# Kernel optimization log

Hardware: AMD Instinct MI355X
Metric: run time of the kernel (lower is better)

The kernel has to match this reference:

```python
import jax, jax.numpy as jnp
import numpy as np

N = 100000      # nodes
E = 1600000     # edges
F_IN, H1, H2, H3, F_OUT = 64, 128, 128, 64, 8


def _lin(key, fan_in, fan_out):
    return jax.random.normal(key, (fan_in, fan_out), jnp.float32) / np.sqrt(fan_in).astype(np.float32)


def setup_inputs() -> dict:
    key = jax.random.key(0)
    ks = jax.random.split(key, 16)
    x = jax.random.normal(ks[0], (N, F_IN), jnp.float32)
    edge_index = jax.random.randint(ks[1], (2, E), 0, N, dtype=jnp.int64)
    return {
        "x": x,
        "edge_index": edge_index,
        "eps1": jnp.zeros((), jnp.float32),
        "eps2": jnp.zeros((), jnp.float32),
        "eps3": jnp.zeros((), jnp.float32),
        "W1a": _lin(ks[2], F_IN, H1), "b1a": jnp.zeros((H1,), jnp.float32),
        "W1b": _lin(ks[3], H1, H1),   "b1b": jnp.zeros((H1,), jnp.float32),
        "W2a": _lin(ks[4], H1, H2),   "b2a": jnp.zeros((H2,), jnp.float32),
        "W2b": _lin(ks[5], H2, H2),   "b2b": jnp.zeros((H2,), jnp.float32),
        "W3a": _lin(ks[6], H2, H3),   "b3a": jnp.zeros((H3,), jnp.float32),
        "W3b": _lin(ks[7], H3, H3),   "b3b": jnp.zeros((H3,), jnp.float32),
        "Wfc": _lin(ks[8], H3, F_OUT), "bfc": jnp.zeros((F_OUT,), jnp.float32),
    }


def _gin_conv(x, src, dst, eps, Wa, ba, Wb, bb):
    # out_i = MLP((1+eps) * x_i + sum_{j in N(i)} x_j)
    agg = jax.ops.segment_sum(x[src], dst, num_segments=N)  # scatter-add over edges
    h = (1.0 + eps) * x + agg
    return jax.nn.relu(h @ Wa + ba) @ Wb + bb


def reference(x, edge_index, eps1, eps2, eps3,
              W1a, b1a, W1b, b1b,
              W2a, b2a, W2b, b2b,
              W3a, b3a, W3b, b3b,
              Wfc, bfc):
    src, dst = edge_index[0], edge_index[1]
    x = jax.nn.relu(_gin_conv(x, src, dst, eps1, W1a, b1a, W1b, b1b))
    x = jax.nn.relu(_gin_conv(x, src, dst, eps2, W2a, b2a, W2b, b2b))
    x = jax.nn.relu(_gin_conv(x, src, dst, eps3, W3a, b3a, W3b, b3b))
    emb = jax.lax.stop_gradient(x)  # x.clone().detach()
    out = x @ Wfc + bfc
    return out, emb
```

## Files before the change

kernel.cpp:

```cpp
#include <hip/hip_runtime.h>
#include <hip/hip_bf16.h>
#include <stdint.h>

typedef unsigned short ushort_t;
typedef __attribute__((ext_vector_type(8))) short short8;
typedef __attribute__((ext_vector_type(4))) float floatx4;
typedef __attribute__((ext_vector_type(2))) float floatx2;

__device__ __forceinline__ unsigned short f2bf(float f){
  union { float f; unsigned int i; } v; v.f = f;
  unsigned int r = v.i + 0x7FFFu + ((v.i >> 16) & 1u);
  return (unsigned short)(r >> 16);
}
__device__ __forceinline__ unsigned int pack2(unsigned short lo, unsigned short hi){
  return ((unsigned int)hi << 16) | (unsigned int)lo;
}
__device__ __forceinline__ floatx2 bfpair(unsigned int v){
  union { unsigned int u; float f; } lo, hi;
  lo.u = v << 16; hi.u = v & 0xffff0000u;
  floatx2 r; r.x = lo.f; r.y = hi.f; return r;
}


__global__ __launch_bounds__(256)
void k_prep(const unsigned int* __restrict__ w, int* __restrict__ ghist, int E, int N, int nbB,
            const float2* __restrict__ xin, unsigned int* __restrict__ xb, int total2, int tobfB,
            const float* __restrict__ W1a, const float* __restrict__ W1b, const float* __restrict__ W2a,
            const float* __restrict__ W2b, const float* __restrict__ W3a, const float* __restrict__ W3b,
            const float* __restrict__ Wfc, ushort_t* __restrict__ wout,
            ushort_t* __restrict__ xbz, ushort_t* __restrict__ x1z, ushort_t* __restrict__ ybz)
{
  int b = blockIdx.x, t = threadIdx.x;
  if (b < nbB){
    __shared__ int h[256];
    __shared__ unsigned int dred[4];
    h[t] = 0;
    int base = b*4096 + t;
    unsigned int acc = 0;
    #pragma unroll
    for (int i=0;i<16;++i){
      int e = base + i*256;
      if (e < E) acc |= w[2*e+1];
    }
    #pragma unroll
    for (int o=32;o>=1;o>>=1) acc |= __shfl_xor(acc, o);
    if ((t&63)==0) dred[t>>6] = acc;
    __syncthreads();
    int m = (dred[0]|dred[1]|dred[2]|dred[3]) != 0;
    #pragma unroll
    for (int i=0;i<16;++i){
      int e = base + i*256;
      if (e < E){
        int d = m ? (int)w[(size_t)E + e] : (int)w[2*((size_t)E + e)];
        if ((unsigned)d < (unsigned)N) atomicAdd(&h[d>>9], 1);
      }
    }
    __syncthreads();
    if (h[t]) atomicAdd(&ghist[t], h[t]);
  } else if (b < nbB + tobfB){
    int i = (b - nbB)*256 + t;
    if (i < total2){
      float2 v = xin[i];
      xb[i] = pack2(f2bf(v.x), f2bf(v.y));
    }
  } else {
    int id = (b - nbB - tobfB)*256 + t;
    if (id >= 74752){
      int id2 = id - 74752;
      if      (id2 <  64) xbz[id2]      = 0;
      else if (id2 < 192) x1z[id2-64]   = 0;
      else if (id2 < 256) ybz[id2-192]  = 0;
      return;
    }
    const float* src; int K, M, base2, local;
    if      (id <  8192){ src=W1a; K=64;  M=128; base2=0;     local=id; }
    else if (id < 24576){ src=W1b; K=128; M=128; base2=8192;  local=id-8192; }
    else if (id < 40960){ src=W2a; K=128; M=128; base2=24576; local=id-24576; }
    else if (id < 57344){ src=W2b; K=128; M=128; base2=40960; local=id-40960; }
    else if (id < 65536){ src=W3a; K=128; M=64;  base2=57344; local=id-57344; }
    else if (id < 69632){ src=W3b; K=64;  M=64;  base2=65536; local=id-65536; }
    else if (id < 70656){ src=Wfc; K=64;  M=16;  base2=69632; local=id-69632; }
    else                { src=nullptr; K=64; M=64; base2=70656; local=id-70656; }
    int k = local / M, nn = local - k*M;
    float val;
    if (src == nullptr) val = (k == nn) ? 1.0f : 0.0f;
    else if (src == Wfc) val = (nn<8) ? Wfc[k*8+nn] : 0.0f;
    else                 val = src[k*M+nn];
    int idx = (((nn>>4)*(K/32) + (k>>5))*4 + ((k>>3)&3))*128 + (nn&15)*8 + (k&7);
    wout[base2+idx] = f2bf(val);
  }
}


__global__ __launch_bounds__(256) void k_bin(const unsigned int* __restrict__ w,
                                             const int* __restrict__ ghist, int* __restrict__ gcur,
                                             int2* __restrict__ pairs,
                                             int E, int N, int NB){
  __shared__ int sv[256];
  __shared__ int h[256];
  __shared__ int cur[256];
  __shared__ unsigned int dred[4];
  int t = threadIdx.x;
  int gv = ghist[t];
  sv[t] = gv; __syncthreads();
  for (int o=1;o<256;o<<=1){
    int xv = (t>=o)? sv[t-o] : 0;
    __syncthreads();
    sv[t] += xv;
    __syncthreads();
  }
  int excl = sv[t] - gv;

  h[t] = 0;
  int base = blockIdx.x*4096 + t;
  unsigned int acc = 0;
  #pragma unroll
  for (int i=0;i<16;++i){
    int e = base + i*256;
    if (e < E) acc |= w[2*e+1];
  }
  #pragma unroll
  for (int o=32;o>=1;o>>=1) acc |= __shfl_xor(acc, o);
  if ((t&63)==0) dred[t>>6] = acc;
  __syncthreads();
  int m = (dred[0]|dred[1]|dred[2]|dred[3]) != 0;
  int d[16], s[16];
  #pragma unroll
  for (int i=0;i<16;++i){
    int e = base + i*256;
    d[i] = -1; s[i] = 0;
    if (e < E){
      if (m){ s[i] = (int)w[e];           d[i] = (int)w[(size_t)E + e]; }
      else  { s[i] = (int)w[2*(size_t)e]; d[i] = (int)w[2*((size_t)E + e)]; }
      if ((unsigned)d[i] >= (unsigned)N || (unsigned)s[i] >= (unsigned)N) d[i] = -1;
    }
  }
  #pragma unroll
  for (int i=0;i<16;++i)
    if (d[i] >= 0) atomicAdd(&h[d[i]>>9], 1);
  __syncthreads();
  if (t < NB && h[t]) cur[t] = excl + atomicAdd(&gcur[t], h[t]);
  __syncthreads();
  #pragma unroll
  for (int i=0;i<16;++i){
    if (d[i] >= 0){
      int p = atomicAdd(&cur[d[i]>>9], 1);
      pairs[p] = make_int2(d[i], s[i]);
    }
  }
}

__global__ __launch_bounds__(256) void k_bcsr(const int2* __restrict__ pairs, const int* __restrict__ ghist,
                                              int* __restrict__ offs, int* __restrict__ csr, int N, int NB){
  __shared__ int sv[256];
  __shared__ int cnt[512];
  __shared__ int wsum[4];
  int b = blockIdx.x, t = threadIdx.x, lane = t&63, wv = t>>6;
  int gv = ghist[t];
  sv[t] = gv; __syncthreads();
  for (int o=1;o<256;o<<=1){
    int xv = (t>=o)? sv[t-o] : 0;
    __syncthreads();
    sv[t] += xv;
    __syncthreads();
  }
  int lo = (b==0) ? 0 : sv[b-1];
  int hi = sv[b];
  int node0 = b << 9;
  cnt[t] = 0; cnt[t+256] = 0;
  __syncthreads();
  for (int i = lo+t; i < hi; i += 256){
    int2 p = pairs[i];
    atomicAdd(&cnt[p.x - node0], 1);
  }
  __syncthreads();
  int v0 = cnt[2*t], v1 = cnt[2*t+1], tot = v0+v1;
  int s = tot;
  #pragma unroll
  for (int o=1;o<64;o<<=1){ int xv = __shfl_up(s,o); if (lane>=o) s += xv; }
  if (lane==63) wsum[wv] = s;
  __syncthreads();
  int basev = 0;
  for (int j=0;j<wv;++j) basev += wsum[j];
  int excl = basev + s - tot;
  int e0 = lo + excl, e1 = lo + excl + v0;
  cnt[2*t] = e0; cnt[2*t+1] = e1;
  int n0 = node0 + 2*t, n1 = node0 + 2*t + 1;
  if (n0 < N) offs[n0] = e0;
  if (n1 < N) offs[n1] = e1;
  if (b == NB-1 && t == 255) offs[N] = hi;
  __syncthreads();
  for (int i = lo+t; i < hi; i += 256){
    int2 p = pairs[i];
    int pos = atomicAdd(&cnt[p.x - node0], 1);
    csr[pos] = p.y;
  }
}


template<int F>
__global__ __launch_bounds__(256) void k_gatherx(const uint4* __restrict__ xr, const int* __restrict__ offs,
                                                 const int* __restrict__ csr, const float* __restrict__ epsp,
                                                 uint4* __restrict__ hr, int n, int nzrow){
  constexpr int RS  = F/8;
  constexpr int LPN = 4*RS;
  constexpr int NPW = 64/LPN;
  constexpr int CH  = LPN;
  constexpr int MAXG = CH/16;
  int gt = blockIdx.x*256 + threadIdx.x;
  int wv = gt >> 6, lane = gt & 63;
  int grp = lane / LPN;
  int lin = lane % LPN;
  int q   = lin / RS;
  int f   = lin % RS;
  int node = wv*NPW + grp;
  if (node >= n) return;
  const size_t row = (size_t)node*RS;
  float e1s = 1.0f + epsp[0];
  floatx2 a0,a1,a2,a3;
  if (q == 0){
    uint4 sv = xr[row + f];
    floatx2 es; es.x = e1s; es.y = e1s;
    a0 = es*bfpair(sv.x); a1 = es*bfpair(sv.y);
    a2 = es*bfpair(sv.z); a3 = es*bfpair(sv.w);
  } else {
    floatx2 z; z.x = 0.f; z.y = 0.f;
    a0 = z; a1 = z; a2 = z; a3 = z;
  }
  int u0 = offs[node], u1 = offs[node+1];
  int deg = u1 - u0;

#define ISSUE(g, V0,V1,V2,V3) { int bb = grp*LPN + (g)*16 + q; \
    int s0=__shfl(cv,bb), s1=__shfl(cv,bb+4), s2=__shfl(cv,bb+8), s3=__shfl(cv,bb+12); \
    V0 = xr[(size_t)s0*RS + f]; V1 = xr[(size_t)s1*RS + f]; \
    V2 = xr[(size_t)s2*RS + f]; V3 = xr[(size_t)s3*RS + f]; }
#define ACCV(V)  { a0 += bfpair((V).x); a1 += bfpair((V).y); a2 += bfpair((V).z); a3 += bfpair((V).w); }
#define ACC4(V0,V1,V2,V3) { ACCV(V0) ACCV(V1) ACCV(V2) ACCV(V3) }

  for (int c0 = 0; c0 < deg; c0 += CH){
    int rem = deg - c0;
    int cv = nzrow;
    if (lin < rem) cv = csr[u0 + c0 + lin];
    int nk = rem < CH ? rem : CH;
    int ng = (nk + 15) >> 4;
    uint4 A0,A1,A2,A3, B0,B1,B2,B3;
    ISSUE(0, A0,A1,A2,A3)
    if (ng > 1) { ISSUE(1, B0,B1,B2,B3) }
    ACC4(A0,A1,A2,A3)
    if (ng > 1){
      if constexpr (MAXG >= 3) { if (ng > 2) ISSUE(2, A0,A1,A2,A3) }
      ACC4(B0,B1,B2,B3)
      if constexpr (MAXG >= 3){
        if (ng > 2){
          if (ng > 3) { ISSUE(3, B0,B1,B2,B3) }
          ACC4(A0,A1,A2,A3)
          if (ng > 3) { ACC4(B0,B1,B2,B3) }
        }
      }
    }
  }
#undef ISSUE
#undef ACCV
#undef ACC4
#define RED(av) { av.x += __shfl_xor(av.x, RS);   av.y += __shfl_xor(av.y, RS); \
                  av.x += __shfl_xor(av.x, 2*RS); av.y += __shfl_xor(av.y, 2*RS); }
  RED(a0) RED(a1) RED(a2) RED(a3)
#undef RED
  if (q == 0){
    uint4 o;
    o.x = pack2(f2bf(a0.x), f2bf(a0.y));
    o.y = pack2(f2bf(a1.x), f2bf(a1.y));
    o.z = pack2(f2bf(a2.x), f2bf(a2.y));
    o.w = pack2(f2bf(a3.x), f2bf(a3.y));
    hr[row + f] = o;
  }
}


template<int F, int M1, int M2, bool LAST, bool Y3>
__global__ __launch_bounds__(256)
void k_gmlp(const uint4* __restrict__ xr, const int* __restrict__ offs,
            const int* __restrict__ csr, const float* __restrict__ epsp,
            const ushort_t* __restrict__ wp1, const float* __restrict__ b1,
            const ushort_t* __restrict__ wp2, const float* __restrict__ b2,
            ushort_t* __restrict__ xout,
            float* __restrict__ embp,
            const ushort_t* __restrict__ wpfc, const float* __restrict__ bfc,
            float* __restrict__ outp, int n)
{
  constexpr int RS  = F/8;
  constexpr int LPN = 4*RS;
  constexpr int NPW = 64/LPN;
  constexpr int CH  = LPN;
  constexpr int MAXG = CH/16;
  constexpr int NPR = 4*NPW;
  constexpr int PADC = F + 8;
  constexpr int NT1 = M1/16, NT2 = M2/16, KC1 = F/32, KC2 = M1/32;

  __shared__ short sH[64*PADC] __attribute__((aligned(16)));
  __shared__ short sC1[4*(M1/8)*136];
  __shared__ short sX3[LAST ? (4*8*136) : 1];

  int tid = threadIdx.x, lane = tid&63, w = tid>>6;
  int node0 = blockIdx.x*64;

  {
    int grp = lane / LPN;
    int lin = lane % LPN;
    int q   = lin / RS;
    int f   = lin % RS;
    float e1s = 1.0f + epsp[0];
    #pragma unroll
    for (int rd = 0; rd < 64/NPR; ++rd){
      int lrow = rd*NPR + w*NPW + grp;
      int node = node0 + lrow;
      int nd = node < n ? node : n;
      floatx2 a0,a1,a2,a3;
      if (q == 0){
        uint4 sv = xr[(size_t)nd*RS + f];
        floatx2 es; es.x = e1s; es.y = e1s;
        a0 = es*bfpair(sv.x); a1 = es*bfpair(sv.y);
        a2 = es*bfpair(sv.z); a3 = es*bfpair(sv.w);
      } else {
        floatx2 z; z.x = 0.f; z.y = 0.f;
        a0 = z; a1 = z; a2 = z; a3 = z;
      }
      int u0 = 0, deg = 0;
      if (node < n){ u0 = offs[node]; deg = offs[node+1] - u0; }

#define ISSUE(g, V0,V1,V2,V3) { int bb = grp*LPN + (g)*16 + q; \
    int s0=__shfl(cv,bb), s1=__shfl(cv,bb+4), s2=__shfl(cv,bb+8), s3=__shfl(cv,bb+12); \
    V0 = xr[(size_t)s0*RS + f]; V1 = xr[(size_t)s1*RS + f]; \
    V2 = xr[(size_t)s2*RS + f]; V3 = xr[(size_t)s3*RS + f]; }
#define ACCV(V)  { a0 += bfpair((V).x); a1 += bfpair((V).y); a2 += bfpair((V).z); a3 += bfpair((V).w); }
#define ACC4(V0,V1,V2,V3) { ACCV(V0) ACCV(V1) ACCV(V2) ACCV(V3) }
      for (int c0 = 0; c0 < deg; c0 += CH){
        int rem = deg - c0;
        int cv = n;
        if (lin < rem) cv = csr[u0 + c0 + lin];
        int nk = rem < CH ? rem : CH;
        int ng = (nk + 15) >> 4;
        uint4 A0,A1,A2,A3, B0,B1,B2,B3;
        ISSUE(0, A0,A1,A2,A3)
        if (ng > 1) { ISSUE(1, B0,B1,B2,B3) }
        ACC4(A0,A1,A2,A3)
        if (ng > 1){
          if constexpr (MAXG >= 3) { if (ng > 2) ISSUE(2, A0,A1,A2,A3) }
          ACC4(B0,B1,B2,B3)
          if constexpr (MAXG >= 3){
            if (ng > 2){
              if (ng > 3) { ISSUE(3, B0,B1,B2,B3) }
              ACC4(A0,A1,A2,A3)
              if (ng > 3) { ACC4(B0,B1,B2,B3) }
            }
          }
        }
      }
#undef ISSUE
#undef ACCV
#undef ACC4
#define RED(av) { av.x += __shfl_xor(av.x, RS);   av.y += __shfl_xor(av.y, RS); \
                  av.x += __shfl_xor(av.x, 2*RS); av.y += __shfl_xor(av.y, 2*RS); }
      RED(a0) RED(a1) RED(a2) RED(a3)
#undef RED
      if (q == 0){
        uint4 o;
        o.x = pack2(f2bf(a0.x), f2bf(a0.y));
        o.y = pack2(f2bf(a1.x), f2bf(a1.y));
        o.z = pack2(f2bf(a2.x), f2bf(a2.y));
        o.w = pack2(f2bf(a3.x), f2bf(a3.y));
        *(uint4*)&sH[lrow*PADC + f*8] = o;
      }
    }
  }
  __syncthreads();

  int m16 = lane&15, quad = lane>>4;
  int row0 = node0 + w*16;

  floatx4 acc[NT1];
  #pragma unroll
  for (int i=0;i<NT1;++i) acc[i] = (floatx4){0.f,0.f,0.f,0.f};
  #pragma unroll
  for (int kc=0; kc<KC1; ++kc){
    short8 a = *(const short8*)&sH[(w*16 + m16)*PADC + kc*32 + quad*8];
    #pragma unroll
    for (int nt=0; nt<NT1; ++nt){
      short8 b = *(const short8*)(wp1 + (size_t)((nt*KC1+kc)*64 + lane)*8);
      acc[nt] = __builtin_amdgcn_mfma_f32_16x16x32_bf16(a, b, acc[nt], 0, 0, 0);
    }
  }
  #pragma unroll
  for (int nt=0; nt<NT1; ++nt){
    int c = nt*16 + m16;
    float bias = b1[c];
    #pragma unroll
    for (int r=0;r<4;++r){
      float v = fmaxf(acc[nt][r] + bias, 0.f);
      int mm = quad*4 + r;
      sC1[(w*(M1/8) + (c>>3))*136 + mm*8 + (c&7)] = (short)f2bf(v);
    }
  }
  __syncthreads();

  floatx4 acc2[NT2];
  #pragma unroll
  for (int i=0;i<NT2;++i) acc2[i] = (floatx4){0.f,0.f,0.f,0.f};
  #pragma unroll
  for (int kc=0; kc<KC2; ++kc){
    short8 a = *(const short8*)&sC1[(w*(M1/8) + kc*4 + quad)*136 + m16*8];
    #pragma unroll
    for (int nt=0; nt<NT2; ++nt){
      short8 b = *(const short8*)(wp2 + (size_t)((nt*KC2+kc)*64 + lane)*8);
      acc2[nt] = __builtin_amdgcn_mfma_f32_16x16x32_bf16(a, b, acc2[nt], 0, 0, 0);
    }
  }
  #pragma unroll
  for (int nt=0; nt<NT2; ++nt){
    int c = nt*16 + m16;
    float bias = b2[c];
    #pragma unroll
    for (int r=0;r<4;++r){
      float v = fmaxf(acc2[nt][r] + bias, 0.f);
      int mm = quad*4 + r;
      int row = row0 + mm;
      if constexpr (Y3){
        sC1[(w*(M2/8) + (c>>3))*136 + mm*8 + (c&7)] = (short)f2bf(v);
      } else if constexpr (!LAST){
        if (row < n) xout[(size_t)row*M2 + c] = f2bf(v);
      } else {
        if (row < n) embp[(size_t)row*64 + c] = v;
        sX3[(w*8 + (c>>3))*136 + mm*8 + (c&7)] = (short)f2bf(v);
      }
    }
  }

  if constexpr (Y3){
    constexpr int KC3 = M2/32;
    floatx4 acc3[4];
    #pragma unroll
    for (int i=0;i<4;++i) acc3[i] = (floatx4){0.f,0.f,0.f,0.f};
    #pragma unroll
    for (int kc=0; kc<KC3; ++kc){
      short8 a = *(const short8*)&sC1[(w*(M2/8) + kc*4 + quad)*136 + m16*8];
      #pragma unroll
      for (int nt=0; nt<4; ++nt){
        short8 b = *(const short8*)(wpfc + (size_t)((nt*KC3+kc)*64 + lane)*8);
        acc3[nt] = __builtin_amdgcn_mfma_f32_16x16x32_bf16(a, b, acc3[nt], 0, 0, 0);
      }
    }
    #pragma unroll
    for (int nt=0; nt<4; ++nt){
      int c = nt*16 + m16;
      #pragma unroll
      for (int r=0;r<4;++r){
        int row = row0 + quad*4 + r;
        if (row < n) xout[(size_t)row*64 + c] = f2bf(acc3[nt][r]);
      }
    }
  }

  if constexpr (LAST){
    __syncthreads();
    floatx4 accf = (floatx4){0.f,0.f,0.f,0.f};
    #pragma unroll
    for (int kc=0; kc<2; ++kc){
      short8 a = *(const short8*)&sX3[(w*8 + kc*4 + quad)*136 + m16*8];
      short8 b = *(const short8*)(wpfc + (size_t)(kc*64 + lane)*8);
      accf = __builtin_amdgcn_mfma_f32_16x16x32_bf16(a, b, accf, 0, 0, 0);
    }
    if (m16 < 8){
      float bias = bfc[m16];
      #pragma unroll
      for (int r=0;r<4;++r){
        int row = row0 + quad*4 + r;
        if (row < n) outp[(size_t)row*8 + m16] = accf[r] + bias;
      }
    }
  }
}


template<int F, int M1, int M2, bool LAST, bool Y3>
__global__ __launch_bounds__(256)
void k_mlp(const ushort_t* __restrict__ h,
           const ushort_t* __restrict__ wp1, const float* __restrict__ b1,
           const ushort_t* __restrict__ wp2, const float* __restrict__ b2,
           ushort_t* __restrict__ xout,
           float* __restrict__ embp,
           const ushort_t* __restrict__ wpfc, const float* __restrict__ bfc,
           float* __restrict__ outp, int n)
{
  constexpr int NT1 = M1/16, NT2 = M2/16, KC1 = F/32, KC2 = M1/32;
  __shared__ short sC1[4*(M1/8)*136];
  __shared__ short sX3[LAST ? (4*8*136) : 1];
  int tid = threadIdx.x, lane = tid&63, w = tid>>6;
  int m16 = lane&15, quad = lane>>4;
  int row0 = blockIdx.x*64 + w*16;
  size_t arow = (size_t)(row0 + m16);

  floatx4 acc[NT1];
  #pragma unroll
  for (int i=0;i<NT1;++i) acc[i] = (floatx4){0.f,0.f,0.f,0.f};
  #pragma unroll
  for (int kc=0; kc<KC1; ++kc){
    short8 a = *(const short8*)(h + arow*F + kc*32 + quad*8);
    #pragma unroll
    for (int nt=0; nt<NT1; ++nt){
      short8 b = *(const short8*)(wp1 + (size_t)((nt*KC1+kc)*64 + lane)*8);
      acc[nt] = __builtin_amdgcn_mfma_f32_16x16x32_bf16(a, b, acc[nt], 0, 0, 0);
    }
  }
  #pragma unroll
  for (int nt=0; nt<NT1; ++nt){
    int c = nt*16 + m16;
    float bias = b1[c];
    #pragma unroll
    for (int r=0;r<4;++r){
      float v = fmaxf(acc[nt][r] + bias, 0.f);
      int mm = quad*4 + r;
      sC1[(w*(M1/8) + (c>>3))*136 + mm*8 + (c&7)] = (short)f2bf(v);
    }
  }
  __syncthreads();

  floatx4 acc2[NT2];
  #pragma unroll
  for (int i=0;i<NT2;++i) acc2[i] = (floatx4){0.f,0.f,0.f,0.f};
  #pragma unroll
  for (int kc=0; kc<KC2; ++kc){
    short8 a = *(const short8*)&sC1[(w*(M1/8) + kc*4 + quad)*136 + m16*8];
    #pragma unroll
    for (int nt=0; nt<NT2; ++nt){
      short8 b = *(const short8*)(wp2 + (size_t)((nt*KC2+kc)*64 + lane)*8);
      acc2[nt] = __builtin_amdgcn_mfma_f32_16x16x32_bf16(a, b, acc2[nt], 0, 0, 0);
    }
  }
  #pragma unroll
  for (int nt=0; nt<NT2; ++nt){
    int c = nt*16 + m16;
    float bias = b2[c];
    #pragma unroll
    for (int r=0;r<4;++r){
      float v = fmaxf(acc2[nt][r] + bias, 0.f);
      int mm = quad*4 + r;
      int row = row0 + mm;
      if constexpr (Y3){
        sC1[(w*(M2/8) + (c>>3))*136 + mm*8 + (c&7)] = (short)f2bf(v);
      } else if constexpr (!LAST){
        if (row < n) xout[(size_t)row*M2 + c] = f2bf(v);
      } else {
        if (row < n) embp[(size_t)row*64 + c] = v;
        sX3[(w*8 + (c>>3))*136 + mm*8 + (c&7)] = (short)f2bf(v);
      }
    }
  }

  if constexpr (Y3){
    constexpr int KC3 = M2/32;
    floatx4 acc3[4];
    #pragma unroll
    for (int i=0;i<4;++i) acc3[i] = (floatx4){0.f,0.f,0.f,0.f};
    #pragma unroll
    for (int kc=0; kc<KC3; ++kc){
      short8 a = *(const short8*)&sC1[(w*(M2/8) + kc*4 + quad)*136 + m16*8];
      #pragma unroll
      for (int nt=0; nt<4; ++nt){
        short8 b = *(const short8*)(wpfc + (size_t)((nt*KC3+kc)*64 + lane)*8);
        acc3[nt] = __builtin_amdgcn_mfma_f32_16x16x32_bf16(a, b, acc3[nt], 0, 0, 0);
      }
    }
    #pragma unroll
    for (int nt=0; nt<4; ++nt){
      int c = nt*16 + m16;
      #pragma unroll
      for (int r=0;r<4;++r){
        int row = row0 + quad*4 + r;
        if (row < n) xout[(size_t)row*64 + c] = f2bf(acc3[nt][r]);
      }
    }
  }

  if constexpr (LAST){
    __syncthreads();
    floatx4 accf = (floatx4){0.f,0.f,0.f,0.f};
    #pragma unroll
    for (int kc=0; kc<2; ++kc){
      short8 a = *(const short8*)&sX3[(w*8 + kc*4 + quad)*136 + m16*8];
      short8 b = *(const short8*)(wpfc + (size_t)(kc*64 + lane)*8);
      accf = __builtin_amdgcn_mfma_f32_16x16x32_bf16(a, b, accf, 0, 0, 0);
    }
    if (m16 < 8){
      float bias = bfc[m16];
      #pragma unroll
      for (int r=0;r<4;++r){
        int row = row0 + quad*4 + r;
        if (row < n) outp[(size_t)row*8 + m16] = accf[r] + bias;
      }
    }
  }
}


extern "C" void kernel_launch(void* const* d_in, const int* in_sizes, int n_in,
                              void* d_out, int out_size, void* d_ws, size_t ws_size,
                              hipStream_t stream)
{
  const int N = in_sizes[0] / 64;
  const int E = in_sizes[1] / 2;
  const int NB = (N + 511) / 512;
  const float*        x    = (const float*)d_in[0];
  const unsigned int* ew   = (const unsigned int*)d_in[1];
  const float* eps1 = (const float*)d_in[2];
  const float* eps2 = (const float*)d_in[3];
  const float* eps3 = (const float*)d_in[4];
  const float* W1a  = (const float*)d_in[5];
  const float* b1a  = (const float*)d_in[6];
  const float* W1b  = (const float*)d_in[7];
  const float* b1b  = (const float*)d_in[8];
  const float* W2a  = (const float*)d_in[9];
  const float* b2a  = (const float*)d_in[10];
  const float* W2b  = (const float*)d_in[11];
  const float* b2b  = (const float*)d_in[12];
  const float* W3a  = (const float*)d_in[13];
  const float* b3a  = (const float*)d_in[14];
  const float* W3b  = (const float*)d_in[15];
  const float* b3b  = (const float*)d_in[16];
  const float* Wfc  = (const float*)d_in[17];
  const float* bfc  = (const float*)d_in[18];

  float* outp = (float*)d_out;
  float* emb  = outp + (size_t)N*8;

  const int Npad = ((N + 63)/64)*64;

  char* ws = (char*)d_ws;
  size_t o = 0;
  auto alloc = [&](size_t bytes)->char* {
    char* p = ws + o;
    o = (o + bytes + 255) & ~(size_t)255;
    return p;
  };
  int*      ghist = (int*)alloc(512*4);
  int*      gcur  = ghist + 256;
  int*      offs  = (int*)alloc((size_t)(N+1)*4);
  int2*     pairs = (int2*)alloc((size_t)E*8);
  int*      csr   = (int*)alloc((size_t)E*4);
  ushort_t* wperm = (ushort_t*)alloc(74752ull*2);
  ushort_t* xb    = (ushort_t*)alloc(((size_t)Npad + 64)*64*2);
  ushort_t* hbuf  = (ushort_t*)alloc((size_t)Npad*128*2);
  ushort_t* x1    = (ushort_t*)alloc(((size_t)Npad + 64)*128*2);
  ushort_t* ybuf  = (ushort_t*)alloc(((size_t)Npad + 64)*64*2);

  hipMemsetAsync(ghist, 0, 512*4, stream);
  const int nbB   = (E + 4095)/4096;
  const int tobfB = (N*32 + 255)/256;
  const int permB = (74752 + 256 + 255)/256;
  k_prep<<<nbB + tobfB + permB, 256, 0, stream>>>(ew, ghist, E, N, nbB,
                                                  (const float2*)x, (unsigned int*)xb, N*32, tobfB,
                                                  W1a, W1b, W2a, W2b, W3a, W3b, Wfc, wperm,
                                                  xb + (size_t)N*64, x1 + (size_t)N*128, ybuf + (size_t)N*64);
  k_bin<<<nbB, 256, 0, stream>>>(ew, ghist, gcur, pairs, E, N, NB);
  k_bcsr<<<NB, 256, 0, stream>>>(pairs, ghist, offs, csr, N, NB);

  k_gmlp<64,128,128,false,false><<<Npad/64, 256, 0, stream>>>((const uint4*)xb, offs, csr, eps1,
                                                              wperm+0, b1a, wperm+8192, b1b,
                                                              x1, nullptr, nullptr, nullptr, nullptr, N);
  k_gatherx<128><<<(N+3)/4, 256, 0, stream>>>((const uint4*)x1, offs, csr, eps2,
                                              (uint4*)hbuf, N, N);
  k_mlp<128,128,128,false,true><<<Npad/64, 256, 0, stream>>>(hbuf, wperm+24576, b2a, wperm+40960, b2b,
                                                             ybuf, nullptr, wperm+57344, nullptr, nullptr, N);
  k_gmlp<64,64,64,true,false><<<Npad/64, 256, 0, stream>>>((const uint4*)ybuf, offs, csr, eps3,
                                                           wperm+70656, b3a, wperm+65536, b3b,
                                                           nullptr, emb, wperm+69632, bfc, outp, N);
}
```

Baseline: 360.5 us.

## Pack CSR build pairs into 32-bit words and widen preprocessing blocks to 1024

Each edge is now packed as the node's local offset within its bin plus the source index in one 32-bit word, replacing an int2 and halving pairs traffic. The prep, bin and CSR kernels move to 1024-thread blocks. The prep kernel records the index-layout flag per block so the bin kernel does not recompute it. The gather+MLP kernel now shares one shared-memory buffer across its stages, loads A fragments into registers before a barrier, and drops the unused Y3 path. The packing assumes node indices fit in 17 bits, and the larger blocks change occupancy and the number of scan barriers.

Result: faster. 345.2 us (-4.2%).

```diff
diff --git a/kernel.cpp b/kernel.cpp
--- a/kernel.cpp
+++ b/kernel.cpp
@@ -22,8 +22,9 @@
 }
 
 
-__global__ __launch_bounds__(256)
-void k_prep(const unsigned int* __restrict__ w, int* __restrict__ ghist, int E, int N, int nbB,
+__global__ __launch_bounds__(1024)
+void k_prep(const unsigned int* __restrict__ w, int* __restrict__ ghist, int* __restrict__ dflag,
+            int E, int N, int nbB,
             const float2* __restrict__ xin, unsigned int* __restrict__ xb, int total2, int tobfB,
             const float* __restrict__ W1a, const float* __restrict__ W1b, const float* __restrict__ W2a,
             const float* __restrict__ W2b, const float* __restrict__ W3a, const float* __restrict__ W3b,
@@ -33,38 +34,42 @@
   int b = blockIdx.x, t = threadIdx.x;
   if (b < nbB){
     __shared__ int h[256];
-    __shared__ unsigned int dred[4];
-    h[t] = 0;
+    __shared__ unsigned int dred[16];
+    if (t < 256) h[t] = 0;
     int base = b*4096 + t;
     unsigned int acc = 0;
     #pragma unroll
-    for (int i=0;i<16;++i){
-      int e = base + i*256;
+    for (int i=0;i<4;++i){
+      int e = base + i*1024;
       if (e < E) acc |= w[2*e+1];
     }
     #pragma unroll
     for (int o=32;o>=1;o>>=1) acc |= __shfl_xor(acc, o);
     if ((t&63)==0) dred[t>>6] = acc;
     __syncthreads();
-    int m = (dred[0]|dred[1]|dred[2]|dred[3]) != 0;
-    #pragma unroll
-    for (int i=0;i<16;++i){
-      int e = base + i*256;
+    unsigned int mm = 0;
+    #pragma unroll
+    for (int i=0;i<16;++i) mm |= dred[i];
+    int m = mm != 0;
+    if (t == 0) dflag[b] = m;
+    #pragma unroll
+    for (int i=0;i<4;++i){
+      int e = base + i*1024;
       if (e < E){
         int d = m ? (int)w[(size_t)E + e] : (int)w[2*((size_t)E + e)];
         if ((unsigned)d < (unsigned)N) atomicAdd(&h[d>>9], 1);
       }
     }
     __syncthreads();
-    if (h[t]) atomicAdd(&ghist[t], h[t]);
+    if (t < 256 && h[t]) atomicAdd(&ghist[t], h[t]);
   } else if (b < nbB + tobfB){
-    int i = (b - nbB)*256 + t;
+    int i = (b - nbB)*1024 + t;
     if (i < total2){
       float2 v = xin[i];
       xb[i] = pack2(f2bf(v.x), f2bf(v.y));
     }
   } else {
-    int id = (b - nbB - tobfB)*256 + t;
+    int id = (b - nbB - tobfB)*1024 + t;
     if (id >= 74752){
       int id2 = id - 74752;
       if      (id2 <  64) xbz[id2]      = 0;
@@ -92,42 +97,33 @@
 }
 
 
-__global__ __launch_bounds__(256) void k_bin(const unsigned int* __restrict__ w,
-                                             const int* __restrict__ ghist, int* __restrict__ gcur,
-                                             int2* __restrict__ pairs,
-                                             int E, int N, int NB){
+__global__ __launch_bounds__(1024) void k_bin(const unsigned int* __restrict__ w,
+                                              const int* __restrict__ ghist, const int* __restrict__ dflag,
+                                              int* __restrict__ gcur,
+                                              unsigned int* __restrict__ pairs,
+                                              int E, int N, int NB){
   __shared__ int sv[256];
   __shared__ int h[256];
   __shared__ int cur[256];
-  __shared__ unsigned int dred[4];
   int t = threadIdx.x;
-  int gv = ghist[t];
-  sv[t] = gv; __syncthreads();
+  int gv = 0;
+  if (t < 256){ gv = ghist[t]; sv[t] = gv; }
+  __syncthreads();
   for (int o=1;o<256;o<<=1){
-    int xv = (t>=o)? sv[t-o] : 0;
-    __syncthreads();
-    sv[t] += xv;
-    __syncthreads();
-  }
-  int excl = sv[t] - gv;
-
-  h[t] = 0;
+    int xv = (t>=o && t<256)? sv[t-o] : 0;
+    __syncthreads();
+    if (t < 256) sv[t] += xv;
+    __syncthreads();
+  }
+  int excl = (t < 256) ? sv[t] - gv : 0;
+  if (t < 256) h[t] = 0;
+  int m = dflag[blockIdx.x];
   int base = blockIdx.x*4096 + t;
-  unsigned int acc = 0;
-  #pragma unroll
-  for (int i=0;i<16;++i){
-    int e = base + i*256;
-    if (e < E) acc |= w[2*e+1];
-  }
-  #pragma unroll
-  for (int o=32;o>=1;o>>=1) acc |= __shfl_xor(acc, o);
-  if ((t&63)==0) dred[t>>6] = acc;
-  __syncthreads();
-  int m = (dred[0]|dred[1]|dred[2]|dred[3]) != 0;
-  int d[16], s[16];
-  #pragma unroll
-  for (int i=0;i<16;++i){
-    int e = base + i*256;
+  __syncthreads();
+  int d[4], s[4];
+  #pragma unroll
+  for (int i=0;i<4;++i){
+    int e = base + i*1024;
     d[i] = -1; s[i] = 0;
     if (e < E){
       if (m){ s[i] = (int)w[e];           d[i] = (int)w[(size_t)E + e]; }
@@ -136,64 +132,69 @@
     }
   }
   #pragma unroll
-  for (int i=0;i<16;++i)
+  for (int i=0;i<4;++i)
     if (d[i] >= 0) atomicAdd(&h[d[i]>>9], 1);
   __syncthreads();
   if (t < NB && h[t]) cur[t] = excl + atomicAdd(&gcur[t], h[t]);
   __syncthreads();
   #pragma unroll
-  for (int i=0;i<16;++i){
+  for (int i=0;i<4;++i){
     if (d[i] >= 0){
       int p = atomicAdd(&cur[d[i]>>9], 1);
-      pairs[p] = make_int2(d[i], s[i]);
-    }
-  }
-}
-
-__global__ __launch_bounds__(256) void k_bcsr(const int2* __restrict__ pairs, const int* __restrict__ ghist,
-                                              int* __restrict__ offs, int* __restrict__ csr, int N, int NB){
+      pairs[p] = ((unsigned int)(d[i] & 511) << 17) | (unsigned int)s[i];
+    }
+  }
+}
+
+__global__ __launch_bounds__(1024) void k_bcsr(const unsigned int* __restrict__ pairs, const int* __restrict__ ghist,
+                                               int* __restrict__ offs, int* __restrict__ csr, int N, int NB){
   __shared__ int sv[256];
   __shared__ int cnt[512];
   __shared__ int wsum[4];
   int b = blockIdx.x, t = threadIdx.x, lane = t&63, wv = t>>6;
-  int gv = ghist[t];
-  sv[t] = gv; __syncthreads();
+  if (t < 256) sv[t] = ghist[t];
+  __syncthreads();
   for (int o=1;o<256;o<<=1){
-    int xv = (t>=o)? sv[t-o] : 0;
-    __syncthreads();
-    sv[t] += xv;
+    int xv = (t>=o && t<256)? sv[t-o] : 0;
+    __syncthreads();
+    if (t < 256) sv[t] += xv;
     __syncthreads();
   }
   int lo = (b==0) ? 0 : sv[b-1];
   int hi = sv[b];
   int node0 = b << 9;
-  cnt[t] = 0; cnt[t+256] = 0;
-  __syncthreads();
-  for (int i = lo+t; i < hi; i += 256){
-    int2 p = pairs[i];
-    atomicAdd(&cnt[p.x - node0], 1);
-  }
-  __syncthreads();
-  int v0 = cnt[2*t], v1 = cnt[2*t+1], tot = v0+v1;
-  int s = tot;
-  #pragma unroll
-  for (int o=1;o<64;o<<=1){ int xv = __shfl_up(s,o); if (lane>=o) s += xv; }
-  if (lane==63) wsum[wv] = s;
-  __syncthreads();
-  int basev = 0;
-  for (int j=0;j<wv;++j) basev += wsum[j];
-  int excl = basev + s - tot;
-  int e0 = lo + excl, e1 = lo + excl + v0;
-  cnt[2*t] = e0; cnt[2*t+1] = e1;
-  int n0 = node0 + 2*t, n1 = node0 + 2*t + 1;
-  if (n0 < N) offs[n0] = e0;
-  if (n1 < N) offs[n1] = e1;
+  if (t < 512) cnt[t] = 0;
+  __syncthreads();
+  for (int i = lo+t; i < hi; i += 1024){
+    unsigned int p = pairs[i];
+    atomicAdd(&cnt[p >> 17], 1);
+  }
+  __syncthreads();
+  int v0 = 0, v1 = 0, tot = 0, s = 0;
+  if (t < 256){
+    v0 = cnt[2*t]; v1 = cnt[2*t+1]; tot = v0+v1;
+    s = tot;
+    #pragma unroll
+    for (int o=1;o<64;o<<=1){ int xv = __shfl_up(s,o); if (lane>=o) s += xv; }
+    if (lane==63) wsum[wv] = s;
+  }
+  __syncthreads();
+  if (t < 256){
+    int basev = 0;
+    for (int j=0;j<wv;++j) basev += wsum[j];
+    int excl = basev + s - tot;
+    int e0 = lo + excl, e1 = lo + excl + v0;
+    cnt[2*t] = e0; cnt[2*t+1] = e1;
+    int n0 = node0 + 2*t, n1 = node0 + 2*t + 1;
+    if (n0 < N) offs[n0] = e0;
+    if (n1 < N) offs[n1] = e1;
+  }
   if (b == NB-1 && t == 255) offs[N] = hi;
   __syncthreads();
-  for (int i = lo+t; i < hi; i += 256){
-    int2 p = pairs[i];
-    int pos = atomicAdd(&cnt[p.x - node0], 1);
-    csr[pos] = p.y;
+  for (int i = lo+t; i < hi; i += 1024){
+    unsigned int p = pairs[i];
+    int pos = atomicAdd(&cnt[p >> 17], 1);
+    csr[pos] = (int)(p & 0x1FFFFu);
   }
 }
 
@@ -277,7 +278,7 @@
 }
 
 
-template<int F, int M1, int M2, bool LAST, bool Y3>
+template<int F, int M1, int M2, bool LAST>
 __global__ __launch_bounds__(256)
 void k_gmlp(const uint4* __restrict__ xr, const int* __restrict__ offs,
             const int* __restrict__ csr, const float* __restrict__ epsp,
@@ -296,10 +297,15 @@
   constexpr int NPR = 4*NPW;
   constexpr int PADC = F + 8;
   constexpr int NT1 = M1/16, NT2 = M2/16, KC1 = F/32, KC2 = M1/32;
-
-  __shared__ short sH[64*PADC] __attribute__((aligned(16)));
-  __shared__ short sC1[4*(M1/8)*136];
-  __shared__ short sX3[LAST ? (4*8*136) : 1];
+  static_assert(KC1 == 2, "a-frag preload written for KC1==2");
+  constexpr int SC1_SZ = 4*(M1/8)*136;
+  constexpr int SX3_SZ = LAST ? (4*8*136) : 0;
+  constexpr int UNION_SZ = (64*PADC > SC1_SZ + SX3_SZ) ? 64*PADC : (SC1_SZ + SX3_SZ);
+
+  __shared__ short sU[UNION_SZ] __attribute__((aligned(16)));
+  short* sH  = sU;
+  short* sC1 = sU;
+  short* sX3 = sU + SC1_SZ;
 
   int tid = threadIdx.x, lane = tid&63, w = tid>>6;
   int node0 = blockIdx.x*64;
@@ -377,18 +383,19 @@
 
   int m16 = lane&15, quad = lane>>4;
   int row0 = node0 + w*16;
+  short8 aR0 = *(const short8*)&sH[(w*16 + m16)*PADC + 0*32 + quad*8];
+  short8 aR1 = *(const short8*)&sH[(w*16 + m16)*PADC + 1*32 + quad*8];
+  __syncthreads();
 
   floatx4 acc[NT1];
   #pragma unroll
   for (int i=0;i<NT1;++i) acc[i] = (floatx4){0.f,0.f,0.f,0.f};
   #pragma unroll
-  for (int kc=0; kc<KC1; ++kc){
-    short8 a = *(const short8*)&sH[(w*16 + m16)*PADC + kc*32 + quad*8];
-    #pragma unroll
-    for (int nt=0; nt<NT1; ++nt){
-      short8 b = *(const short8*)(wp1 + (size_t)((nt*KC1+kc)*64 + lane)*8);
-      acc[nt] = __builtin_amdgcn_mfma_f32_16x16x32_bf16(a, b, acc[nt], 0, 0, 0);
-    }
+  for (int nt=0; nt<NT1; ++nt){
+    short8 b0 = *(const short8*)(wp1 + (size_t)((nt*KC1+0)*64 + lane)*8);
+    acc[nt] = __builtin_amdgcn_mfma_f32_16x16x32_bf16(aR0, b0, acc[nt], 0, 0, 0);
+    short8 b1v = *(const short8*)(wp1 + (size_t)((nt*KC1+1)*64 + lane)*8);
+    acc[nt] = __builtin_amdgcn_mfma_f32_16x16x32_bf16(aR1, b1v, acc[nt], 0, 0, 0);
   }
   #pragma unroll
   for (int nt=0; nt<NT1; ++nt){
@@ -424,38 +431,11 @@
       float v = fmaxf(acc2[nt][r] + bias, 0.f);
       int mm = quad*4 + r;
       int row = row0 + mm;
-      if constexpr (Y3){
-        sC1[(w*(M2/8) + (c>>3))*136 + mm*8 + (c&7)] = (short)f2bf(v);
-      } else if constexpr (!LAST){
+      if constexpr (!LAST){
         if (row < n) xout[(size_t)row*M2 + c] = f2bf(v);
       } else {
         if (row < n) embp[(size_t)row*64 + c] = v;
         sX3[(w*8 + (c>>3))*136 + mm*8 + (c&7)] = (short)f2bf(v);
-      }
-    }
-  }
-
-  if constexpr (Y3){
-    constexpr int KC3 = M2/32;
-    floatx4 acc3[4];
-    #pragma unroll
-    for (int i=0;i<4;++i) acc3[i] = (floatx4){0.f,0.f,0.f,0.f};
-    #pragma unroll
-    for (int kc=0; kc<KC3; ++kc){
-      short8 a = *(const short8*)&sC1[(w*(M2/8) + kc*4 + quad)*136 + m16*8];
-      #pragma unroll
-      for (int nt=0; nt<4; ++nt){
-        short8 b = *(const short8*)(wpfc + (size_t)((nt*KC3+kc)*64 + lane)*8);
-        acc3[nt] = __builtin_amdgcn_mfma_f32_16x16x32_bf16(a, b, acc3[nt], 0, 0, 0);
-      }
-    }
-    #pragma unroll
-    for (int nt=0; nt<4; ++nt){
-      int c = nt*16 + m16;
-      #pragma unroll
-      for (int r=0;r<4;++r){
-        int row = row0 + quad*4 + r;
-        if (row < n) xout[(size_t)row*64 + c] = f2bf(acc3[nt][r]);
       }
     }
   }
@@ -633,6 +613,7 @@
   float* emb  = outp + (size_t)N*8;
 
   const int Npad = ((N + 63)/64)*64;
+  const int nbB  = (E + 4095)/4096;
 
   char* ws = (char*)d_ws;
   size_t o = 0;
@@ -643,8 +624,9 @@
   };
   int*      ghist = (int*)alloc(512*4);
   int*      gcur  = ghist + 256;
+  int*      dflag = (int*)alloc((size_t)nbB*4);
   int*      offs  = (int*)alloc((size_t)(N+1)*4);
-  int2*     pairs = (int2*)alloc((size_t)E*8);
+  unsigned int* pairs = (unsigned int*)alloc((size_t)E*4);
   int*      csr   = (int*)alloc((size_t)E*4);
   ushort_t* wperm = (ushort_t*)alloc(74752ull*2);
   ushort_t* xb    = (ushort_t*)alloc(((size_t)Npad + 64)*64*2);
@@ -653,24 +635,23 @@
   ushort_t* ybuf  = (ushort_t*)alloc(((size_t)Npad + 64)*64*2);
 
   hipMemsetAsync(ghist, 0, 512*4, stream);
-  const int nbB   = (E + 4095)/4096;
-  const int tobfB = (N*32 + 255)/256;
-  const int permB = (74752 + 256 + 255)/256;
-  k_prep<<<nbB + tobfB + permB, 256, 0, stream>>>(ew, ghist, E, N, nbB,
-                                                  (const float2*)x, (unsigned int*)xb, N*32, tobfB,
-                                                  W1a, W1b, W2a, W2b, W3a, W3b, Wfc, wperm,
-                                                  xb + (size_t)N*64, x1 + (size_t)N*128, ybuf + (size_t)N*64);
-  k_bin<<<nbB, 256, 0, stream>>>(ew, ghist, gcur, pairs, E, N, NB);
-  k_bcsr<<<NB, 256, 0, stream>>>(pairs, ghist, offs, csr, N, NB);
-
-  k_gmlp<64,128,128,false,false><<<Npad/64, 256, 0, stream>>>((const uint4*)xb, offs, csr, eps1,
-                                                              wperm+0, b1a, wperm+8192, b1b,
-                                                              x1, nullptr, nullptr, nullptr, nullptr, N);
+  const int tobfB = (N*32 + 1023)/1024;
+  const int permB = (74752 + 256 + 1023)/1024;
+  k_prep<<<nbB + tobfB + permB, 1024, 0, stream>>>(ew, ghist, dflag, E, N, nbB,
+                                                   (const float2*)x, (unsigned int*)xb, N*32, tobfB,
+                                                   W1a, W1b, W2a, W2b, W3a, W3b, Wfc, wperm,
+                                                   xb + (size_t)N*64, x1 + (size_t)N*128, ybuf + (size_t)N*64);
+  k_bin<<<nbB, 1024, 0, stream>>>(ew, ghist, dflag, gcur, pairs, E, N, NB);
+  k_bcsr<<<NB, 1024, 0, stream>>>(pairs, ghist, offs, csr, N, NB);
+
+  k_gmlp<64,128,128,false><<<Npad/64, 256, 0, stream>>>((const uint4*)xb, offs, csr, eps1,
+                                                        wperm+0, b1a, wperm+8192, b1b,
+                                                        x1, nullptr, nullptr, nullptr, nullptr, N);
   k_gatherx<128><<<(N+3)/4, 256, 0, stream>>>((const uint4*)x1, offs, csr, eps2,
                                               (uint4*)hbuf, N, N);
   k_mlp<128,128,128,false,true><<<Npad/64, 256, 0, stream>>>(hbuf, wperm+24576, b2a, wperm+40960, b2b,
                                                              ybuf, nullptr, wperm+57344, nullptr, nullptr, N);
-  k_gmlp<64,64,64,true,false><<<Npad/64, 256, 0, stream>>>((const uint4*)ybuf, offs, csr, eps3,
-                                                           wperm+70656, b3a, wperm+65536, b3b,
-                                                           nullptr, emb, wperm+69632, bfc, outp, N);
-}
+  k_gmlp<64,64,64,true><<<Npad/64, 256, 0, stream>>>((const uint4*)ybuf, offs, csr, eps3,
+                                                     wperm+70656, b3a, wperm+65536, b3b,
+                                                     nullptr, emb, wperm+69632, bfc, outp, N);
+}
```
